# Optimization experiments

Measured on AMD Instinct MI355X. Metric: run time of the kernel, lower is better.

The kernel has to match this reference:

```python
import jax, jax.numpy as jnp
import numpy as np

NUM_SINK = 8  # cfg.SINKHORN_ITERS


def _sinkhorn_log(c, log_a, log_b, lambd):
    # c: [M+1, N+1] augmented coupling scores (sinkhorn_unrolled: log_p = -c/lambd)
    log_p = -c / lambd
    for _ in range(NUM_SINK):  # fixed small unroll, matches num_sink
        log_p = log_p - (jax.nn.logsumexp(log_p, axis=-2, keepdims=True) - log_b[None, :])
        log_p = log_p - (jax.nn.logsumexp(log_p, axis=-1, keepdims=True) - log_a[:, None])
    return jnp.exp(log_p)


def setup_inputs() -> dict:
    key = jax.random.key(0)
    k1, k2 = jax.random.split(key)
    G, M, N, D = 128, 512, 512, 512
    return {
        "det_feats": jax.random.normal(k1, (G, N, D), dtype=jnp.float32),
        "tra_feats": jax.random.normal(k2, (G, M, D), dtype=jnp.float32),
        "alpha": jnp.ones((1,), dtype=jnp.float32),
        "eplison": jnp.zeros((1,), dtype=jnp.float32),
    }


def reference(det_feats, tra_feats, alpha, eplison):
    G, N, D = det_feats.shape
    M = tra_feats.shape[1]
    # cosine affinity per graph: [G, M, N]
    corr = jnp.einsum('gmd,gnd->gmn', tra_feats, det_feats)
    n1 = jnp.linalg.norm(tra_feats, axis=-1)  # [G, M]
    n2 = jnp.linalg.norm(det_feats, axis=-1)  # [G, N]
    affinity = corr / (n1[:, :, None] * n2[:, None, :])
    a = alpha[0]
    bins0 = jnp.broadcast_to(a, (G, M, 1)).astype(affinity.dtype)
    bins1 = jnp.broadcast_to(a, (G, 1, N)).astype(affinity.dtype)
    corner = jnp.broadcast_to(a, (G, 1, 1)).astype(affinity.dtype)
    couplings = jnp.concatenate([
        jnp.concatenate([affinity, bins0], axis=-1),
        jnp.concatenate([bins1, corner], axis=-1),
    ], axis=-2)  # [G, M+1, N+1]
    norm = 1.0 / (M + N)
    a_aug = jnp.full((M + 1,), norm, dtype=jnp.float32).at[-1].set(norm * N)
    b_aug = jnp.full((N + 1,), norm, dtype=jnp.float32).at[-1].set(norm * M)
    log_a = jnp.log(a_aug)
    log_b = jnp.log(b_aug)
    lambd = jnp.exp(eplison[0]) + 0.03
    pred = jax.vmap(lambda c: _sinkhorn_log(c, log_a, log_b, lambd))(couplings)
    return pred  # [G, M+1, N+1]
```

## Files before the change

### kernel.cpp

```cpp
#include <hip/hip_runtime.h>
#include <hip/hip_bf16.h>

#define G    128
#define MDIM 512
#define NDIM 512
#define DDIM 512
#define NORMC 0.0009765625f
#define BINW  0.5f
#define PW   516

using short8 = __attribute__((ext_vector_type(8))) short;
using short4v = __attribute__((ext_vector_type(4))) short;
using f32x4 = __attribute__((ext_vector_type(4))) float;

__device__ inline float bf2f(unsigned short u) {
    unsigned int x = ((unsigned int)u) << 16;
    return __builtin_bit_cast(float, x);
}
__device__ inline unsigned short f2bf(float f) {
    return __builtin_bit_cast(unsigned short, __float2bfloat16(f));
}
__device__ inline short4v cvt4(float4 f) {
    short4v r;
    r[0] = __builtin_bit_cast(short, __float2bfloat16(f.x));
    r[1] = __builtin_bit_cast(short, __float2bfloat16(f.y));
    r[2] = __builtin_bit_cast(short, __float2bfloat16(f.z));
    r[3] = __builtin_bit_cast(short, __float2bfloat16(f.w));
    return r;
}

__global__ __launch_bounds__(256)
void gt_cvt_kernel(const float* __restrict__ tra, const float* __restrict__ det,
                   unsigned short* __restrict__ trab, unsigned short* __restrict__ detb)
{
    int wave = threadIdx.x >> 6, lane = threadIdx.x & 63;
    long row0 = ((long)blockIdx.x * 4 + wave) * 4;
    const long per = (long)G * MDIM;
    const float* src; unsigned short* dst; long r0;
    if (row0 < per) { src = tra; dst = trab; r0 = row0; }
    else            { src = det; dst = detb; r0 = row0 - per; }
    float4 x0[4], x1[4];
    #pragma unroll
    for (int r = 0; r < 4; ++r) {
        const float4* p = reinterpret_cast<const float4*>(src + (size_t)(r0 + r) * DDIM);
        x0[r] = p[lane * 2];
        x1[r] = p[lane * 2 + 1];
    }
    float s[4];
    #pragma unroll
    for (int r = 0; r < 4; ++r)
        s[r] = x0[r].x*x0[r].x + x0[r].y*x0[r].y + x0[r].z*x0[r].z + x0[r].w*x0[r].w
             + x1[r].x*x1[r].x + x1[r].y*x1[r].y + x1[r].z*x1[r].z + x1[r].w*x1[r].w;
    #pragma unroll
    for (int off = 1; off < 64; off <<= 1) {
        #pragma unroll
        for (int r = 0; r < 4; ++r) s[r] += __shfl_xor(s[r], off);
    }
    #pragma unroll
    for (int r = 0; r < 4; ++r) {
        float rs = rsqrtf(s[r]);
        short4v lo = cvt4(make_float4(x0[r].x*rs, x0[r].y*rs, x0[r].z*rs, x0[r].w*rs));
        short4v hi = cvt4(make_float4(x1[r].x*rs, x1[r].y*rs, x1[r].z*rs, x1[r].w*rs));
        short8 o;
        o[0]=lo[0]; o[1]=lo[1]; o[2]=lo[2]; o[3]=lo[3];
        o[4]=hi[0]; o[5]=hi[1]; o[6]=hi[2]; o[7]=hi[3];
        *reinterpret_cast<short8*>(dst + (size_t)(r0 + r) * 512 + lane * 8) = o;
    }
}

__global__ __launch_bounds__(256)
void gt_gemm_bf16(const unsigned short* __restrict__ trab, const unsigned short* __restrict__ detb,
                  const float* __restrict__ eps,
                  unsigned short* __restrict__ Ke, float* __restrict__ P1)
{
    __shared__ short As[128 * 40];
    __shared__ short Bs[128 * 40];
    int bid = blockIdx.x;
    int xcd = bid & 7, slot = bid >> 3;
    int g = xcd * 16 + (slot >> 4);
    int tile = slot & 15;
    int tm = tile >> 2, tn = tile & 3;
    int t = threadIdx.x, lane = t & 63, wave = t >> 6;
    int wr = wave >> 1, wc = wave & 1;
    f32x4 acc[4][4] = {};
    const unsigned short* Ab = trab + ((size_t)g << 18) + (size_t)(tm * 128) * 512;
    const unsigned short* Bb = detb + ((size_t)g << 18) + (size_t)(tn * 128) * 512;
    int srow = t >> 2;
    int sslot = t & 3;

    for (int kt = 0; kt < 16; ++kt) {
        int k0 = kt * 32;
        #pragma unroll
        for (int p = 0; p < 2; ++p) {
            int row = p * 64 + srow;
            short8 a = *reinterpret_cast<const short8*>(Ab + (size_t)row * 512 + k0 + sslot * 8);
            short8 b = *reinterpret_cast<const short8*>(Bb + (size_t)row * 512 + k0 + sslot * 8);
            *reinterpret_cast<short8*>(&As[row * 40 + sslot * 8]) = a;
            *reinterpret_cast<short8*>(&Bs[row * 40 + sslot * 8]) = b;
        }
        __syncthreads();
        short8 af[4], bfv[4];
        #pragma unroll
        for (int i = 0; i < 4; ++i) {
            int arow = wr * 64 + i * 16 + (lane & 15);
            af[i]  = *reinterpret_cast<const short8*>(&As[arow * 40 + (lane >> 4) * 8]);
            int brow = wc * 64 + i * 16 + (lane & 15);
            bfv[i] = *reinterpret_cast<const short8*>(&Bs[brow * 40 + (lane >> 4) * 8]);
        }
        #pragma unroll
        for (int i = 0; i < 4; ++i)
            #pragma unroll
            for (int j = 0; j < 4; ++j)
                acc[i][j] = __builtin_amdgcn_mfma_f32_16x16x32_bf16(af[i], bfv[j], acc[i][j], 0, 0, 0);
        __syncthreads();
    }

    float lam = __expf(eps[0]) + 0.03f;
    float nscale = -1.0f / lam;
    size_t kbase = (size_t)g << 18;
    int r0v = (lane >> 4) * 4;
    int c0 = lane & 15;
    #pragma unroll
    for (int j = 0; j < 4; ++j) {
        int lcol = wc * 64 + j * 16 + c0;
        int colg = tn * 128 + lcol;
        float cacc = 0.f;
        #pragma unroll
        for (int i = 0; i < 4; ++i) {
            int lrow = wr * 64 + i * 16 + r0v;
            #pragma unroll
            for (int r = 0; r < 4; ++r) {
                float ev = __expf(acc[i][j][r] * nscale);
                cacc += ev;
                int rowg = tm * 128 + lrow + r;
                Ke[kbase + (size_t)rowg * 512 + colg] = f2bf(ev);
            }
        }
        cacc += __shfl_down(cacc, 32);
        cacc += __shfl_down(cacc, 16);
        if (lane < 16)
            P1[(size_t)g * (8 * PW) + (size_t)(2 * tm + wr) * PW + tn * 128 + wc * 64 + j * 16 + lane] = cacc;
    }
}

__global__ __launch_bounds__(256)
void gt_gemm_legacy(const float* __restrict__ tra, const float* __restrict__ det,
                    const float* __restrict__ eps,
                    float* __restrict__ Koutf, float* __restrict__ P1)
{
    __shared__ short As[128 * 40];
    __shared__ short Bs[128 * 40];
    __shared__ float rnA[128];
    __shared__ float rnB[128];
    int bid = blockIdx.x;
    int xcd = bid & 7, slot = bid >> 3;
    int g = xcd * 16 + (slot >> 4);
    int tile = slot & 15;
    int tm = tile >> 2, tn = tile & 3;
    int t = threadIdx.x, lane = t & 63, wave = t >> 6;
    int wr = wave >> 1, wc = wave & 1;
    f32x4 acc[4][4] = {};
    const float* Abase = tra + (size_t)g * MDIM * DDIM + (size_t)(tm * 128) * DDIM;
    const float* Bbase = det + (size_t)g * NDIM * DDIM + (size_t)(tn * 128) * DDIM;
    int srow = t >> 3, scol = t & 7;
    float ssA[4] = {0.f, 0.f, 0.f, 0.f};
    float ssB[4] = {0.f, 0.f, 0.f, 0.f};

    for (int kt = 0; kt < 16; ++kt) {
        int k0 = kt * 32;
        #pragma unroll
        for (int p = 0; p < 4; ++p) {
            int row = p * 32 + srow;
            float4 a = *reinterpret_cast<const float4*>(Abase + (size_t)row * DDIM + k0 + scol * 4);
            float4 b = *reinterpret_cast<const float4*>(Bbase + (size_t)row * DDIM + k0 + scol * 4);
            ssA[p] += a.x*a.x + a.y*a.y + a.z*a.z + a.w*a.w;
            ssB[p] += b.x*b.x + b.y*b.y + b.z*b.z + b.w*b.w;
            *reinterpret_cast<short4v*>(&As[row * 40 + scol * 4]) = cvt4(a);
            *reinterpret_cast<short4v*>(&Bs[row * 40 + scol * 4]) = cvt4(b);
        }
        __syncthreads();
        short8 af[4], bfv[4];
        #pragma unroll
        for (int i = 0; i < 4; ++i) {
            int arow = wr * 64 + i * 16 + (lane & 15);
            af[i]  = *reinterpret_cast<const short8*>(&As[arow * 40 + (lane >> 4) * 8]);
            int brow = wc * 64 + i * 16 + (lane & 15);
            bfv[i] = *reinterpret_cast<const short8*>(&Bs[brow * 40 + (lane >> 4) * 8]);
        }
        #pragma unroll
        for (int i = 0; i < 4; ++i)
            #pragma unroll
            for (int j = 0; j < 4; ++j)
                acc[i][j] = __builtin_amdgcn_mfma_f32_16x16x32_bf16(af[i], bfv[j], acc[i][j], 0, 0, 0);
        __syncthreads();
    }

    #pragma unroll
    for (int p = 0; p < 4; ++p) {
        float a = ssA[p], b = ssB[p];
        a += __shfl_xor(a, 1); a += __shfl_xor(a, 2); a += __shfl_xor(a, 4);
        b += __shfl_xor(b, 1); b += __shfl_xor(b, 2); b += __shfl_xor(b, 4);
        if (scol == 0) { rnA[p * 32 + srow] = rsqrtf(a); rnB[p * 32 + srow] = rsqrtf(b); }
    }
    __syncthreads();

    float lam = __expf(eps[0]) + 0.03f;
    float nscale = -1.0f / lam;
    size_t obase = (size_t)g * 263169;
    int r0v = (lane >> 4) * 4;
    int c0 = lane & 15;
    #pragma unroll
    for (int j = 0; j < 4; ++j) {
        int lcol = wc * 64 + j * 16 + c0;
        int colg = tn * 128 + lcol;
        float sc2 = nscale * rnB[lcol];
        float cacc = 0.f;
        #pragma unroll
        for (int i = 0; i < 4; ++i) {
            int lrow = wr * 64 + i * 16 + r0v;
            #pragma unroll
            for (int r = 0; r < 4; ++r) {
                float ev = __expf(acc[i][j][r] * rnA[lrow + r] * sc2);
                cacc += ev;
                int rowg = tm * 128 + lrow + r;
                Koutf[obase + (size_t)rowg * 513 + colg] = ev;
            }
        }
        cacc += __shfl_down(cacc, 32);
        cacc += __shfl_down(cacc, 16);
        if (lane < 16)
            P1[(size_t)g * (8 * PW) + (size_t)(2 * tm + wr) * PW + tn * 128 + wc * 64 + j * 16 + lane] = cacc;
    }
}

template<bool BF16, bool LAST>
__global__ __launch_bounds__(512)
void gt_iter(const void* __restrict__ Kv,
             const float* __restrict__ alpha, const float* __restrict__ eps,
             const float* __restrict__ Pread, float* __restrict__ Pwrite,
             float* __restrict__ outp, int first, int writeP)
{
    __shared__ float bv_s[512];
    __shared__ float colpart[8][512];
    __shared__ float rtmp[8];
    __shared__ float scal[2];
    int g = blockIdx.y, rb = blockIdx.x;
    int t = threadIdx.x, lane = t & 63, wv = t >> 6;
    float lam = __expf(eps[0]) + 0.03f;
    float val = __expf(-alpha[0] / lam);
    const float* Pg = Pread + (size_t)g * (8 * PW);
    float au512p = first ? 1.0f : Pg[513];
    float cs = 0.f;
    #pragma unroll
    for (int b = 0; b < 8; ++b) cs += Pg[b * PW + t];
    float bvt = NORMC / (cs + val * au512p);
    bv_s[t] = bvt;
    float sb = bvt;
    #pragma unroll
    for (int off = 1; off < 64; off <<= 1) sb += __shfl_xor(sb, off);
    if (lane == 0) rtmp[wv] = sb;
    __syncthreads();
    if (t == 0) {
        float S_bv = 0.f;
        #pragma unroll
        for (int w = 0; w < 8; ++w) S_bv += rtmp[w];
        float S_au_prev;
        if (first) S_au_prev = 513.f;
        else { float s = 0.f; for (int b = 0; b < 8; ++b) s += Pg[b * PW + 512]; S_au_prev = s + au512p; }
        float bv512 = BINW / (val * S_au_prev);
        float au512n = BINW / (val * (S_bv + bv512));
        scal[0] = bv512;
        scal[1] = au512n;
        if (!LAST && rb == 0) Pwrite[(size_t)g * (8 * PW) + 513] = au512n;
    }
    __syncthreads();
    float bv512 = scal[0];

    float bvr[8];
    #pragma unroll
    for (int k = 0; k < 8; ++k) bvr[k] = bv_s[lane * 8 + k];
    float colacc[8] = {};
    float suma = 0.f;
    const size_t RS = BF16 ? 512 : 513;
    size_t base = BF16 ? ((size_t)g << 18) : ((size_t)g * 263169);
    size_t obase = (size_t)g * 263169;
    int rowbase = rb * 64;
    for (int rr = wv; rr < 64; rr += 8) {
        int r = rowbase + rr;
        float kv[8];
        if constexpr (BF16) {
            short8 x = *reinterpret_cast<const short8*>((const unsigned short*)Kv + base + (size_t)r * RS + lane * 8);
            #pragma unroll
            for (int k = 0; k < 8; ++k) kv[k] = bf2f((unsigned short)x[k]);
        } else {
            const float* p = (const float*)Kv + base + (size_t)r * RS + lane * 8;
            #pragma unroll
            for (int k = 0; k < 8; ++k) kv[k] = p[k];
        }
        float dot = 0.f;
        #pragma unroll
        for (int k = 0; k < 8; ++k) dot += kv[k] * bvr[k];
        #pragma unroll
        for (int off = 1; off < 64; off <<= 1) dot += __shfl_xor(dot, off);
        float au_r = NORMC / (dot + val * bv512);
        if constexpr (LAST) {
            float* orow = outp + obase + (size_t)r * 513;
            f32x4 o0, o1;
            #pragma unroll
            for (int k = 0; k < 4; ++k) {
                o0[k] = kv[k] * au_r * bvr[k];
                o1[k] = kv[4 + k] * au_r * bvr[4 + k];
            }
            *reinterpret_cast<f32x4*>(orow + lane * 8)     = o0;
            *reinterpret_cast<f32x4*>(orow + lane * 8 + 4) = o1;
            if (lane == 0) orow[512] = val * au_r * bv512;
        } else {
            suma += au_r;
            #pragma unroll
            for (int k = 0; k < 8; ++k) colacc[k] += kv[k] * au_r;
        }
    }
    if constexpr (LAST) {
        if (rb == 7) {
            float au512n = scal[1];
            float* brow = outp + obase + (size_t)512 * 513;
            brow[t] = val * au512n * bv_s[t];
            if (t == 0) brow[512] = val * au512n * bv512;
        }
    } else if (writeP) {
        #pragma unroll
        for (int k = 0; k < 8; ++k) colpart[wv][lane * 8 + k] = colacc[k];
        if (lane == 0) rtmp[wv] = suma;
        __syncthreads();
        float s0 = 0.f;
        #pragma unroll
        for (int w = 0; w < 8; ++w) s0 += colpart[w][t];
        float* Pw = Pwrite + (size_t)g * (8 * PW) + (size_t)rb * PW;
        Pw[t] = s0;
        if (t == 0) {
            float ss = 0.f;
            #pragma unroll
            for (int w = 0; w < 8; ++w) ss += rtmp[w];
            Pw[512] = ss;
        }
    }
}

extern "C" void kernel_launch(void* const* d_in, const int* in_sizes, int n_in,
                              void* d_out, int out_size, void* d_ws, size_t ws_size,
                              hipStream_t stream) {
    const float* det   = (const float*)d_in[0];
    const float* tra   = (const float*)d_in[1];
    const float* alpha = (const float*)d_in[2];
    const float* eps   = (const float*)d_in[3];
    float* out = (float*)d_out;

    float* P0 = (float*)d_ws;
    float* P1 = P0 + (size_t)G * 8 * PW;
    unsigned short* ke = (unsigned short*)(P1 + (size_t)G * 8 * PW);

    size_t smallBytes = (size_t)2 * G * 8 * PW * 4;
    bool fast = ws_size >= smallBytes + ((size_t)G << 19);

    if (fast) {
        unsigned short* trab = (unsigned short*)out;
        unsigned short* detb = trab + ((size_t)G << 18);
        gt_cvt_kernel<<<(2 * G * MDIM) / 16, 256, 0, stream>>>(tra, det, trab, detb);
        gt_gemm_bf16<<<2048, 256, 0, stream>>>(trab, detb, eps, ke, P1);
        float* Pr = P1; float* Pw = P0;
        for (int it = 0; it < 7; ++it) {
            gt_iter<true, false><<<dim3(8, G), 512, 0, stream>>>((const void*)ke, alpha, eps, Pr, Pw, nullptr, it == 0 ? 1 : 0, 1);
            float* tmp = Pr; Pr = Pw; Pw = tmp;
        }
        gt_iter<true, true><<<dim3(8, G), 512, 0, stream>>>((const void*)ke, alpha, eps, Pr, Pw, out, 0, 0);
    } else {
        gt_gemm_legacy<<<2048, 256, 0, stream>>>(tra, det, eps, out, P1);
        float* Pr = P1; float* Pw = P0;
        for (int it = 0; it < 7; ++it) {
            gt_iter<false, false><<<dim3(8, G), 512, 0, stream>>>((const void*)out, alpha, eps, Pr, Pw, nullptr, it == 0 ? 1 : 0, 1);
            float* tmp = Pr; Pr = Pw; Pw = tmp;
        }
        gt_iter<false, true><<<dim3(8, G), 512, 0, stream>>>((const void*)out, alpha, eps, Pr, Pw, out, 0, 0);
    }
}
```

Before: 286.1 us.

## Store the exp kernel matrix in custom FP8 e4m3-like format for Sinkhorn iterations

The exponentiated coupling matrix K is now stored as one byte per entry using a hand-rolled exponent/mantissa encoding instead of bf16. This halves the bytes each of the eight Sinkhorn iteration kernels reads, and the workspace requirement for the fast path drops accordingly. The GEMM epilogue accumulates column sums from the dequantized values so they stay consistent with what the iterations read. The conversion kernel is also reshaped to handle two rows per wave with twice as many blocks. The 3-bit mantissa loses a lot of precision, and the custom encoding maps very small exp values incorrectly, which risks accuracy.

```diff
diff --git a/kernel.cpp b/kernel.cpp
--- a/kernel.cpp
+++ b/kernel.cpp
@@ -28,50 +28,60 @@
     r[3] = __builtin_bit_cast(short, __float2bfloat16(f.w));
     return r;
 }
+__device__ inline unsigned char f2e4m3(float f) {
+    unsigned int b = __builtin_bit_cast(unsigned int, f);
+    unsigned int t = b + 0x7FFFFu + ((b >> 20) & 1u);
+    return (unsigned char)((t >> 20) - 960u);
+}
+__device__ inline float e4m32f(unsigned int u) {
+    return __builtin_bit_cast(float, (u << 20) + 0x3C000000u);
+}
 
 __global__ __launch_bounds__(256)
 void gt_cvt_kernel(const float* __restrict__ tra, const float* __restrict__ det,
                    unsigned short* __restrict__ trab, unsigned short* __restrict__ detb)
 {
     int wave = threadIdx.x >> 6, lane = threadIdx.x & 63;
-    long row0 = ((long)blockIdx.x * 4 + wave) * 4;
+    long row0 = (long)blockIdx.x * 8 + wave * 2;
     const long per = (long)G * MDIM;
     const float* src; unsigned short* dst; long r0;
     if (row0 < per) { src = tra; dst = trab; r0 = row0; }
     else            { src = det; dst = detb; r0 = row0 - per; }
-    float4 x0[4], x1[4];
-    #pragma unroll
-    for (int r = 0; r < 4; ++r) {
-        const float4* p = reinterpret_cast<const float4*>(src + (size_t)(r0 + r) * DDIM);
-        x0[r] = p[lane * 2];
-        x1[r] = p[lane * 2 + 1];
-    }
-    float s[4];
-    #pragma unroll
-    for (int r = 0; r < 4; ++r)
-        s[r] = x0[r].x*x0[r].x + x0[r].y*x0[r].y + x0[r].z*x0[r].z + x0[r].w*x0[r].w
-             + x1[r].x*x1[r].x + x1[r].y*x1[r].y + x1[r].z*x1[r].z + x1[r].w*x1[r].w;
+    const float4* p0 = reinterpret_cast<const float4*>(src + r0 * DDIM);
+    const float4* p1 = reinterpret_cast<const float4*>(src + (r0 + 1) * DDIM);
+    float4 a0 = p0[lane * 2], a1 = p0[lane * 2 + 1];
+    float4 b0 = p1[lane * 2], b1 = p1[lane * 2 + 1];
+    float sa = a0.x*a0.x + a0.y*a0.y + a0.z*a0.z + a0.w*a0.w
+             + a1.x*a1.x + a1.y*a1.y + a1.z*a1.z + a1.w*a1.w;
+    float sb = b0.x*b0.x + b0.y*b0.y + b0.z*b0.z + b0.w*b0.w
+             + b1.x*b1.x + b1.y*b1.y + b1.z*b1.z + b1.w*b1.w;
     #pragma unroll
     for (int off = 1; off < 64; off <<= 1) {
-        #pragma unroll
-        for (int r = 0; r < 4; ++r) s[r] += __shfl_xor(s[r], off);
-    }
-    #pragma unroll
-    for (int r = 0; r < 4; ++r) {
-        float rs = rsqrtf(s[r]);
-        short4v lo = cvt4(make_float4(x0[r].x*rs, x0[r].y*rs, x0[r].z*rs, x0[r].w*rs));
-        short4v hi = cvt4(make_float4(x1[r].x*rs, x1[r].y*rs, x1[r].z*rs, x1[r].w*rs));
-        short8 o;
-        o[0]=lo[0]; o[1]=lo[1]; o[2]=lo[2]; o[3]=lo[3];
-        o[4]=hi[0]; o[5]=hi[1]; o[6]=hi[2]; o[7]=hi[3];
-        *reinterpret_cast<short8*>(dst + (size_t)(r0 + r) * 512 + lane * 8) = o;
-    }
+        sa += __shfl_xor(sa, off);
+        sb += __shfl_xor(sb, off);
+    }
+    float ra = rsqrtf(sa), rb = rsqrtf(sb);
+    short8 oa, ob;
+    {
+        short4v lo = cvt4(make_float4(a0.x*ra, a0.y*ra, a0.z*ra, a0.w*ra));
+        short4v hi = cvt4(make_float4(a1.x*ra, a1.y*ra, a1.z*ra, a1.w*ra));
+        oa[0]=lo[0]; oa[1]=lo[1]; oa[2]=lo[2]; oa[3]=lo[3];
+        oa[4]=hi[0]; oa[5]=hi[1]; oa[6]=hi[2]; oa[7]=hi[3];
+    }
+    {
+        short4v lo = cvt4(make_float4(b0.x*rb, b0.y*rb, b0.z*rb, b0.w*rb));
+        short4v hi = cvt4(make_float4(b1.x*rb, b1.y*rb, b1.z*rb, b1.w*rb));
+        ob[0]=lo[0]; ob[1]=lo[1]; ob[2]=lo[2]; ob[3]=lo[3];
+        ob[4]=hi[0]; ob[5]=hi[1]; ob[6]=hi[2]; ob[7]=hi[3];
+    }
+    *reinterpret_cast<short8*>(dst + (size_t)r0 * 512 + lane * 8)       = oa;
+    *reinterpret_cast<short8*>(dst + (size_t)(r0 + 1) * 512 + lane * 8) = ob;
 }
 
 __global__ __launch_bounds__(256)
 void gt_gemm_bf16(const unsigned short* __restrict__ trab, const unsigned short* __restrict__ detb,
                   const float* __restrict__ eps,
-                  unsigned short* __restrict__ Ke, float* __restrict__ P1)
+                  unsigned char* __restrict__ Ke, float* __restrict__ P1)
 {
     __shared__ short As[128 * 40];
     __shared__ short Bs[128 * 40];
@@ -131,9 +141,9 @@
             #pragma unroll
             for (int r = 0; r < 4; ++r) {
                 float ev = __expf(acc[i][j][r] * nscale);
-                cacc += ev;
-                int rowg = tm * 128 + lrow + r;
-                Ke[kbase + (size_t)rowg * 512 + colg] = f2bf(ev);
+                unsigned char q = f2e4m3(ev);
+                Ke[kbase + (size_t)(tm * 128 + lrow + r) * 512 + colg] = q;
+                cacc += e4m32f(q);
             }
         }
         cacc += __shfl_down(cacc, 32);
@@ -233,7 +243,7 @@
     }
 }
 
-template<bool BF16, bool LAST>
+template<bool FP8, bool LAST>
 __global__ __launch_bounds__(512)
 void gt_iter(const void* __restrict__ Kv,
              const float* __restrict__ alpha, const float* __restrict__ eps,
@@ -281,19 +291,24 @@
     for (int k = 0; k < 8; ++k) bvr[k] = bv_s[lane * 8 + k];
     float colacc[8] = {};
     float suma = 0.f;
-    const size_t RS = BF16 ? 512 : 513;
-    size_t base = BF16 ? ((size_t)g << 18) : ((size_t)g * 263169);
+    size_t base = FP8 ? ((size_t)g << 18) : ((size_t)g * 263169);
     size_t obase = (size_t)g * 263169;
     int rowbase = rb * 64;
     for (int rr = wv; rr < 64; rr += 8) {
         int r = rowbase + rr;
         float kv[8];
-        if constexpr (BF16) {
-            short8 x = *reinterpret_cast<const short8*>((const unsigned short*)Kv + base + (size_t)r * RS + lane * 8);
-            #pragma unroll
-            for (int k = 0; k < 8; ++k) kv[k] = bf2f((unsigned short)x[k]);
+        if constexpr (FP8) {
+            uint2 w = *reinterpret_cast<const uint2*>((const unsigned char*)Kv + base + (size_t)r * 512 + lane * 8);
+            kv[0] = e4m32f(w.x & 255u);
+            kv[1] = e4m32f((w.x >> 8) & 255u);
+            kv[2] = e4m32f((w.x >> 16) & 255u);
+            kv[3] = e4m32f(w.x >> 24);
+            kv[4] = e4m32f(w.y & 255u);
+            kv[5] = e4m32f((w.y >> 8) & 255u);
+            kv[6] = e4m32f((w.y >> 16) & 255u);
+            kv[7] = e4m32f(w.y >> 24);
         } else {
-            const float* p = (const float*)Kv + base + (size_t)r * RS + lane * 8;
+            const float* p = (const float*)Kv + base + (size_t)r * 513 + lane * 8;
             #pragma unroll
             for (int k = 0; k < 8; ++k) kv[k] = p[k];
         }
@@ -357,15 +372,15 @@
 
     float* P0 = (float*)d_ws;
     float* P1 = P0 + (size_t)G * 8 * PW;
-    unsigned short* ke = (unsigned short*)(P1 + (size_t)G * 8 * PW);
+    unsigned char* ke = (unsigned char*)(P1 + (size_t)G * 8 * PW);
 
     size_t smallBytes = (size_t)2 * G * 8 * PW * 4;
-    bool fast = ws_size >= smallBytes + ((size_t)G << 19);
+    bool fast = ws_size >= smallBytes + ((size_t)G << 18);
 
     if (fast) {
         unsigned short* trab = (unsigned short*)out;
         unsigned short* detb = trab + ((size_t)G << 18);
-        gt_cvt_kernel<<<(2 * G * MDIM) / 16, 256, 0, stream>>>(tra, det, trab, detb);
+        gt_cvt_kernel<<<(2 * G * MDIM) / 8, 256, 0, stream>>>(tra, det, trab, detb);
         gt_gemm_bf16<<<2048, 256, 0, stream>>>(trab, detb, eps, ke, P1);
         float* Pr = P1; float* Pw = P0;
         for (int it = 0; it < 7; ++it) {
```

After: 273.3 us (median of 2 runs). -4.5%, faster.
